# Kernel optimization log

Hardware: AMD Instinct MI355X
Metric: run time of the kernel (lower is better)

## Reference

```python
import jax, jax.numpy as jnp
import numpy as np

B, C, W, H = 32, 512, 28, 28  # input spatial = 2*init_width x 2*init_height
HEADS = 8


def setup_inputs() -> dict:
    key = jax.random.key(0)
    ks = jax.random.split(key, 9)
    d = C // HEADS
    s = 0.05
    return {
        "x": jax.random.normal(ks[0], (B, C, W, H), jnp.float32),
        # 1x1 conv weights == dense [out_c, in_c] + bias
        "wq": jax.random.normal(ks[1], (C, C), jnp.float32) * s,
        "bq": jax.random.normal(ks[2], (C,), jnp.float32) * s,
        "wk": jax.random.normal(ks[3], (C, C), jnp.float32) * s,
        "bk": jax.random.normal(ks[4], (C,), jnp.float32) * s,
        "wv": jax.random.normal(ks[5], (C, C), jnp.float32) * s,
        "bv": jax.random.normal(ks[6], (C,), jnp.float32) * s,
        "rel_h": jax.random.normal(ks[7], (1, HEADS, d, 1, H), jnp.float32),
        "rel_w": jax.random.normal(ks[8], (1, HEADS, d, W, 1), jnp.float32),
    }


def reference(x, wq, bq, wk, bk, wv, bv, rel_h, rel_w):
    b, c, w, h = x.shape
    heads = rel_h.shape[1]
    d = c // heads
    n = w * h

    def proj(wt, bi):
        # 1x1 conv == per-pixel dense over channels
        y = jnp.einsum('oc,bcwh->bowh', wt, x) + bi[None, :, None, None]
        return y.reshape(b, heads, d, n)  # [B, H, d, N]

    q = proj(wq, bq)
    k = proj(wk, bk)
    v = proj(wv, bv)

    # content-content: q^T k -> [B, H, N, N]
    cc = jnp.einsum('bhdn,bhdm->bhnm', q, k)
    # relative position bias: (rel_h + rel_w) broadcast to [H, d, 2w0*2h0] = [H, d, N]
    pos = (rel_h + rel_w).reshape(heads, d, n)
    # content-position: pos^T @ q -> [B, H, N, N]
    cp = jnp.einsum('hdp,bhdn->bhpn', pos, q)

    attn = jax.nn.softmax(cc + cp, axis=-1)  # softmax over last dim
    # out = v @ attn^T : [B, H, d, N]
    out = jnp.einsum('bhdn,bhmn->bhdm', v, attn)
    return out.reshape(b, c, w, h)
```

## Files before the change

### kernel.cpp

```cpp
#include <hip/hip_runtime.h>


#define BATCH 32
#define CCH   512
#define NHEAD 8
#define DH    64
#define NTOK  784
#define WSP   28
#define OT    128
#define NT    112
#define WLD   40
#define CH    64
#define NCHUNK 13
#define NIBLK  7
#define KQLD  136
#define VLD   72

typedef unsigned short u16;
typedef unsigned int   u32;
typedef short  short8  __attribute__((ext_vector_type(8)));
typedef float  floatx4 __attribute__((ext_vector_type(4)));

__device__ __forceinline__ u16 f2bf(float f) {
    union { float f; u32 i; } v; v.f = f;
    u32 x = v.i;
    return (u16)((x + 0x7FFFu + ((x >> 16) & 1u)) >> 16);
}
__device__ __forceinline__ u32 f2u(float f) { union { float f; u32 i; } v; v.f = f; return v.i; }
__device__ __forceinline__ float u2f(u32 u) { union { u32 i; float f; } v; v.i = u; return v.f; }

__device__ __forceinline__ u32 packsplit(float f) {
    const u32 hib = f2u(f) & 0xFFFF0000u;
    const float lo = f - u2f(hib);
    return ((u32)f2bf(lo) << 16) | (hib >> 16);
}

__global__ __launch_bounds__(256)
void pack_weights(const float* __restrict__ wq, const float* __restrict__ wk,
                  const float* __restrict__ wv,
                  u32* __restrict__ Wqp, u32* __restrict__ Wkp, u32* __restrict__ Wvp)
{
    const int i = blockIdx.x * 256 + threadIdx.x;
    if (i < CCH * CCH) {
        Wqp[i] = packsplit(wq[i]);
        Wkp[i] = packsplit(wk[i]);
        Wvp[i] = packsplit(wv[i]);
    }
}

__global__ __launch_bounds__(256)
void pack_x(const float* __restrict__ x, u32* __restrict__ Xp, int b0, size_t count)
{
    const size_t i = (size_t)blockIdx.x * 256 + threadIdx.x;
    if (i < count)
        Xp[i] = packsplit(x[(size_t)b0 * CCH * NTOK + i]);
}

__global__ __launch_bounds__(512, 4)
void qkv_proj(const u32* __restrict__ Xp,
              const u32* __restrict__ Wqp, const float* __restrict__ bq,
              const u32* __restrict__ Wkp, const float* __restrict__ bk,
              const u32* __restrict__ Wvp, const float* __restrict__ bv,
              u32* __restrict__ Qp, u32* __restrict__ Kp, u16* __restrict__ Vo,
              int nbatch)
{
    const int t    = threadIdx.x;
    const int lane = t & 63;
    const int wid  = t >> 6;
    const int z    = blockIdx.z;
    const int proj = z / nbatch;
    const int bl   = z - proj * nbatch;
    const int o0   = blockIdx.y * OT;
    const int n0   = blockIdx.x * NT;

    const u32*   Wp   = (proj == 0) ? Wqp : (proj == 1) ? Wkp : Wvp;
    const float* bias = (proj == 0) ? bq  : (proj == 1) ? bk  : bv;

    __shared__ u16 wh[OT][WLD], wl[OT][WLD];
    __shared__ u16 xh[NT][WLD], xl[NT][WLD];

    const int m    = lane & 15;
    const int quad = lane >> 4;

    floatx4 acc[7];
    #pragma unroll
    for (int j = 0; j < 7; j++) acc[j] = (floatx4){0.f, 0.f, 0.f, 0.f};

    const int wo = t >> 2;
    const int wc = (t & 3) * 8;
    const int xc = t >> 3;
    const int xn = (t & 7) * 14;

    const size_t xbase = (size_t)bl * CCH * NTOK;

    uint4 wv0, wv1;
    u32 xreg[14];
    {
        wv0 = *reinterpret_cast<const uint4*>(&Wp[(size_t)(o0 + wo) * CCH + 0 + wc]);
        wv1 = *reinterpret_cast<const uint4*>(&Wp[(size_t)(o0 + wo) * CCH + 0 + wc + 4]);
        if (t < 256) {
            #pragma unroll
            for (int u = 0; u < 7; u++) {
                const uint2 p = *reinterpret_cast<const uint2*>(&Xp[xbase + (size_t)(0 + xc) * NTOK + n0 + xn + 2 * u]);
                xreg[2 * u] = p.x; xreg[2 * u + 1] = p.y;
            }
        }
    }

    for (int c0 = 0; c0 < CCH; c0 += 32) {
        __syncthreads();
        {
            const u32 wr[8] = {wv0.x, wv0.y, wv0.z, wv0.w, wv1.x, wv1.y, wv1.z, wv1.w};
            ushort4 h0 = make_ushort4((u16)(wr[0] & 0xFFFF), (u16)(wr[1] & 0xFFFF), (u16)(wr[2] & 0xFFFF), (u16)(wr[3] & 0xFFFF));
            ushort4 h1 = make_ushort4((u16)(wr[4] & 0xFFFF), (u16)(wr[5] & 0xFFFF), (u16)(wr[6] & 0xFFFF), (u16)(wr[7] & 0xFFFF));
            ushort4 l0 = make_ushort4((u16)(wr[0] >> 16), (u16)(wr[1] >> 16), (u16)(wr[2] >> 16), (u16)(wr[3] >> 16));
            ushort4 l1 = make_ushort4((u16)(wr[4] >> 16), (u16)(wr[5] >> 16), (u16)(wr[6] >> 16), (u16)(wr[7] >> 16));
            *reinterpret_cast<ushort4*>(&wh[wo][wc])     = h0;
            *reinterpret_cast<ushort4*>(&wh[wo][wc + 4]) = h1;
            *reinterpret_cast<ushort4*>(&wl[wo][wc])     = l0;
            *reinterpret_cast<ushort4*>(&wl[wo][wc + 4]) = l1;
        }
        if (t < 256) {
            #pragma unroll
            for (int u = 0; u < 14; u++) {
                xh[xn + u][xc] = (u16)(xreg[u] & 0xFFFFu);
                xl[xn + u][xc] = (u16)(xreg[u] >> 16);
            }
        }
        __syncthreads();

        if (c0 + 32 < CCH) {
            wv0 = *reinterpret_cast<const uint4*>(&Wp[(size_t)(o0 + wo) * CCH + c0 + 32 + wc]);
            wv1 = *reinterpret_cast<const uint4*>(&Wp[(size_t)(o0 + wo) * CCH + c0 + 32 + wc + 4]);
            if (t < 256) {
                #pragma unroll
                for (int u = 0; u < 7; u++) {
                    const uint2 p = *reinterpret_cast<const uint2*>(&Xp[xbase + (size_t)(c0 + 32 + xc) * NTOK + n0 + xn + 2 * u]);
                    xreg[2 * u] = p.x; xreg[2 * u + 1] = p.y;
                }
            }
        }
        __builtin_amdgcn_sched_barrier(0);

        const short8 Ah = *reinterpret_cast<const short8*>(&wh[wid * 16 + m][quad * 8]);
        const short8 Al = *reinterpret_cast<const short8*>(&wl[wid * 16 + m][quad * 8]);
        #pragma unroll
        for (int jt = 0; jt < 7; jt++) {
            const short8 Bh = *reinterpret_cast<const short8*>(&xh[jt * 16 + m][quad * 8]);
            const short8 Bl = *reinterpret_cast<const short8*>(&xl[jt * 16 + m][quad * 8]);
            acc[jt] = __builtin_amdgcn_mfma_f32_16x16x32_bf16(Ah, Bh, acc[jt], 0, 0, 0);
            acc[jt] = __builtin_amdgcn_mfma_f32_16x16x32_bf16(Ah, Bl, acc[jt], 0, 0, 0);
            acc[jt] = __builtin_amdgcn_mfma_f32_16x16x32_bf16(Al, Bh, acc[jt], 0, 0, 0);
        }
    }

    const size_t obase = (size_t)bl * CCH * NTOK;
    #pragma unroll
    for (int r = 0; r < 4; r++) {
        const int o = o0 + wid * 16 + quad * 4 + r;
        const float bi = bias[o];
        #pragma unroll
        for (int jt = 0; jt < 7; jt++) {
            const int n = n0 + jt * 16 + m;
            const float val = acc[jt][r] + bi;
            const size_t idx = obase + (size_t)o * NTOK + n;
            if (proj == 0)      Qp[idx] = packsplit(val);
            else if (proj == 1) Kp[idx] = packsplit(val);
            else                Vo[idx] = f2bf(val);
        }
    }
}

__global__ __launch_bounds__(512)
void attn_kernel(const u32* __restrict__ Qp, const u32* __restrict__ Kp,
                 const u16* __restrict__ V,
                 const float* __restrict__ rel_h, const float* __restrict__ rel_w,
                 float* __restrict__ out, int b0)
{
    const int t    = threadIdx.x;
    const int lane = t & 63;
    const int wid  = t >> 6;
    const int m    = lane & 15;
    const int quad = lane >> 4;
    const int bl   = blockIdx.x;
    const int h    = blockIdx.y;
    int i0 = blockIdx.z * 128;
    if (i0 > NTOK - 128) i0 = NTOK - 128;
    const int b  = b0 + bl;
    const int hd = h * DH;
    const size_t base  = ((size_t)bl * CCH + hd) * NTOK;
    const size_t baseo = ((size_t)b  * CCH + hd) * NTOK;

    __shared__ u16 kqh[CH][KQLD];
    __shared__ u16 kql[CH][KQLD];
    __shared__ u16 vt[DH][VLD];
    __shared__ u16 pt[128][VLD];

    short8 Bh[4], Bl[4];
    {
        const int ig = i0 + wid * 16 + m;
        const int iw = ig / WSP, ih = ig % WSP;
        #pragma unroll
        for (int c = 0; c < 4; c++) {
            union { short8 v; u16 u[8]; } hb, lb;
            #pragma unroll
            for (int idx = 0; idx < 8; idx++) {
                const int k = c * 32 + quad * 8 + idx;
                if (k < DH) {
                    const u32 p = Qp[base + (size_t)k * NTOK + ig];
                    hb.u[idx] = (u16)(p & 0xFFFFu);
                    lb.u[idx] = (u16)(p >> 16);
                } else {
                    const int d = k - DH;
                    const float pos = rel_h[(size_t)(hd + d) * WSP + ih]
                                    + rel_w[(size_t)(hd + d) * WSP + iw];
                    const u32 hib = f2u(pos) & 0xFFFF0000u;
                    hb.u[idx] = (u16)(hib >> 16);
                    lb.u[idx] = f2bf(pos - u2f(hib));
                }
            }
            Bh[c] = hb.v; Bl[c] = lb.v;
        }
    }

    floatx4 Oacc[4];
    #pragma unroll
    for (int dt = 0; dt < 4; dt++) Oacc[dt] = (floatx4){0.f, 0.f, 0.f, 0.f};
    float mrun = -1e30f, lrun = 0.f;

    const int cg4 = (t & 31) * 4;
    const int jb4 = (t >> 5) * 4;
    const int vd  = t >> 3;
    const int vj  = (t & 7) * 8;

    for (int chn = 0; chn < NCHUNK; chn++) {
        const int j0 = chn * CH;
        __syncthreads();

        {
            u32 kv[4][4];
            #pragma unroll
            for (int cc = 0; cc < 4; cc++) {
                const int c = cg4 + cc;
                const u32* src = (c < DH) ? (Kp + base + (size_t)c * NTOK)
                                          : (Qp + base + (size_t)(c - DH) * NTOK);
                const uint4 a = *reinterpret_cast<const uint4*>(&src[j0 + jb4]);
                kv[cc][0] = a.x; kv[cc][1] = a.y; kv[cc][2] = a.z; kv[cc][3] = a.w;
            }
            #pragma unroll
            for (int jj = 0; jj < 4; jj++) {
                const ushort4 hi = make_ushort4((u16)(kv[0][jj] & 0xFFFFu), (u16)(kv[1][jj] & 0xFFFFu),
                                                (u16)(kv[2][jj] & 0xFFFFu), (u16)(kv[3][jj] & 0xFFFFu));
                const ushort4 lo = make_ushort4((u16)(kv[0][jj] >> 16), (u16)(kv[1][jj] >> 16),
                                                (u16)(kv[2][jj] >> 16), (u16)(kv[3][jj] >> 16));
                *reinterpret_cast<ushort4*>(&kqh[jb4 + jj][cg4]) = hi;
                *reinterpret_cast<ushort4*>(&kql[jb4 + jj][cg4]) = lo;
            }
        }
        if (j0 + vj + 8 <= NTOK) {
            const uint4 a = *reinterpret_cast<const uint4*>(&V[base + (size_t)vd * NTOK + j0 + vj]);
            *reinterpret_cast<uint4*>(&vt[vd][vj]) = a;
        } else {
            #pragma unroll
            for (int u = 0; u < 8; u++)
                vt[vd][vj + u] = (j0 + vj + u < NTOK) ? V[base + (size_t)vd * NTOK + j0 + vj + u] : (u16)0;
        }
        __syncthreads();

        floatx4 Sacc[4];
        #pragma unroll
        for (int js = 0; js < 4; js++) Sacc[js] = (floatx4){0.f, 0.f, 0.f, 0.f};
        #pragma unroll
        for (int c = 0; c < 4; c++) {
            #pragma unroll
            for (int js = 0; js < 4; js++) {
                const short8 Ah = *reinterpret_cast<const short8*>(&kqh[js * 16 + m][c * 32 + quad * 8]);
                const short8 Al = *reinterpret_cast<const short8*>(&kql[js * 16 + m][c * 32 + quad * 8]);
                Sacc[js] = __builtin_amdgcn_mfma_f32_16x16x32_bf16(Ah, Bh[c], Sacc[js], 0, 0, 0);
                Sacc[js] = __builtin_amdgcn_mfma_f32_16x16x32_bf16(Ah, Bl[c], Sacc[js], 0, 0, 0);
                Sacc[js] = __builtin_amdgcn_mfma_f32_16x16x32_bf16(Al, Bh[c], Sacc[js], 0, 0, 0);
            }
        }

        float sv[16];
        #pragma unroll
        for (int js = 0; js < 4; js++)
            #pragma unroll
            for (int r = 0; r < 4; r++) sv[js * 4 + r] = Sacc[js][r];
        if (j0 + CH > NTOK) {
            #pragma unroll
            for (int js = 0; js < 4; js++)
                #pragma unroll
                for (int r = 0; r < 4; r++)
                    if (j0 + js * 16 + quad * 4 + r >= NTOK) sv[js * 4 + r] = -1e30f;
        }
        float mc = sv[0];
        #pragma unroll
        for (int u = 1; u < 16; u++) mc = fmaxf(mc, sv[u]);
        mc = fmaxf(mc, __shfl_xor(mc, 16, 64));
        mc = fmaxf(mc, __shfl_xor(mc, 32, 64));
        const float mnew  = fmaxf(mrun, mc);
        const float alpha = __expf(mrun - mnew);
        float ps = 0.f;
        #pragma unroll
        for (int u = 0; u < 16; u++) {
            const float p = __expf(sv[u] - mnew);
            sv[u] = p;
            ps += p;
        }
        ps += __shfl_xor(ps, 16, 64);
        ps += __shfl_xor(ps, 32, 64);
        lrun = lrun * alpha + ps;
        mrun = mnew;
        #pragma unroll
        for (int dt = 0; dt < 4; dt++)
            #pragma unroll
            for (int r = 0; r < 4; r++) Oacc[dt][r] *= alpha;

        #pragma unroll
        for (int js = 0; js < 4; js++) {
            const ushort4 pw = make_ushort4(f2bf(sv[js * 4 + 0]), f2bf(sv[js * 4 + 1]),
                                            f2bf(sv[js * 4 + 2]), f2bf(sv[js * 4 + 3]));
            *reinterpret_cast<ushort4*>(&pt[wid * 16 + m][js * 16 + quad * 4]) = pw;
        }

        #pragma unroll
        for (int joff = 0; joff < CH; joff += 32) {
            const short8 Bp = *reinterpret_cast<const short8*>(&pt[wid * 16 + m][joff + quad * 8]);
            #pragma unroll
            for (int dt = 0; dt < 4; dt++) {
                const short8 Av = *reinterpret_cast<const short8*>(&vt[dt * 16 + m][joff + quad * 8]);
                Oacc[dt] = __builtin_amdgcn_mfma_f32_16x16x32_bf16(Av, Bp, Oacc[dt], 0, 0, 0);
            }
        }
    }

    const float linv = 1.f / lrun;
    #pragma unroll
    for (int dt = 0; dt < 4; dt++) {
        #pragma unroll
        for (int r = 0; r < 4; r++) {
            const int d = dt * 16 + quad * 4 + r;
            out[baseo + (size_t)d * NTOK + i0 + wid * 16 + m] = Oacc[dt][r] * linv;
        }
    }
}

extern "C" void kernel_launch(void* const* d_in, const int* in_sizes, int n_in,
                              void* d_out, int out_size, void* d_ws, size_t ws_size,
                              hipStream_t stream)
{
    const float* x  = (const float*)d_in[0];
    const float* wq = (const float*)d_in[1];
    const float* bq = (const float*)d_in[2];
    const float* wk = (const float*)d_in[3];
    const float* bk = (const float*)d_in[4];
    const float* wv = (const float*)d_in[5];
    const float* bv = (const float*)d_in[6];
    const float* rh = (const float*)d_in[7];
    const float* rw = (const float*)d_in[8];
    float* out = (float*)d_out;

    const size_t perB = (size_t)CCH * NTOK;
    const size_t WELEM = (size_t)CCH * CCH;
    const size_t weightBytes = 3 * WELEM * 4;
    const size_t perBatchBytes = perB * 14;

    size_t avail = (ws_size > weightBytes) ? (ws_size - weightBytes) : perBatchBytes;
    size_t nb_s = avail / perBatchBytes;
    int nb = (int)(nb_s < 1 ? 1 : (nb_s > BATCH ? BATCH : nb_s));

    u32* Wqp = (u32*)d_ws;
    u32* Wkp = Wqp + WELEM;
    u32* Wvp = Wkp + WELEM;
    u32* chunk0 = Wvp + WELEM;

    pack_weights<<<dim3((CCH * CCH + 255) / 256), dim3(256), 0, stream>>>(wq, wk, wv, Wqp, Wkp, Wvp);

    for (int b0 = 0; b0 < BATCH; b0 += nb) {
        const int curb = (BATCH - b0 < nb) ? (BATCH - b0) : nb;
        u32* Xp = chunk0;
        u32* Qp = Xp + (size_t)curb * perB;
        u32* Kp = Qp + (size_t)curb * perB;
        u16* Vb = (u16*)(Kp + (size_t)curb * perB);

        const size_t xcount = (size_t)curb * perB;
        pack_x<<<dim3((unsigned)((xcount + 255) / 256)), dim3(256), 0, stream>>>(x, Xp, b0, xcount);

        dim3 gp(NTOK / NT, CCH / OT, 3 * curb);
        qkv_proj<<<gp, dim3(512), 0, stream>>>(Xp, Wqp, bq, Wkp, bk, Wvp, bv,
                                               Qp, Kp, Vb, curb);

        dim3 ga(curb, NHEAD, NIBLK);
        attn_kernel<<<ga, dim3(512), 0, stream>>>(Qp, Kp, Vb, rh, rw, out, b0);
    }
}
```

Before: 525.6 us.

## Transpose packed X to token-major layout and skip low-weight MFMA for V

The X packing kernel now transposes x into an [N, C] token-major layout through a shared-memory tile. This lets the projection kernel load X with wide 16-byte vectors per row and write LDS with vector stores instead of scattered 2-byte stores. For the V projection, the weight low-part term (Al*Bh) and its LDS staging are skipped, since V is stored in bf16 anyway. This reduces MFMA count and LDS traffic for a third of the blocks, at the cost of slightly lower V precision and a transpose step in the pack kernel.

```diff
diff --git a/kernel.cpp b/kernel.cpp
--- a/kernel.cpp
+++ b/kernel.cpp
@@ -49,15 +49,38 @@
 }
 
 __global__ __launch_bounds__(256)
-void pack_x(const float* __restrict__ x, u32* __restrict__ Xp, int b0, size_t count)
+void pack_xt(const float* __restrict__ x, u32* __restrict__ Xt, int b0)
 {
-    const size_t i = (size_t)blockIdx.x * 256 + threadIdx.x;
-    if (i < count)
-        Xp[i] = packsplit(x[(size_t)b0 * CCH * NTOK + i]);
+    const int bl = blockIdx.z;
+    const int c0 = blockIdx.y * 32;
+    const int n0 = blockIdx.x * 32;
+    const int t  = threadIdx.x;
+    const int tn = t & 31;
+    const int tr = t >> 5;
+
+    __shared__ float tile[32][33];
+
+    const size_t xb = (size_t)(b0 + bl) * CCH * NTOK;
+    #pragma unroll
+    for (int k = 0; k < 4; k++) {
+        const int c = tr + k * 8;
+        const int n = n0 + tn;
+        if (n < NTOK)
+            tile[c][tn] = x[xb + (size_t)(c0 + c) * NTOK + n];
+    }
+    __syncthreads();
+    const size_t ob = (size_t)bl * NTOK * CCH;
+    #pragma unroll
+    for (int k = 0; k < 4; k++) {
+        const int n = n0 + tr + k * 8;
+        const int c = c0 + tn;
+        if (n < NTOK)
+            Xt[ob + (size_t)n * CCH + c] = packsplit(tile[tn][tr + k * 8]);
+    }
 }
 
 __global__ __launch_bounds__(512, 4)
-void qkv_proj(const u32* __restrict__ Xp,
+void qkv_proj(const u32* __restrict__ Xt,
               const u32* __restrict__ Wqp, const float* __restrict__ bq,
               const u32* __restrict__ Wkp, const float* __restrict__ bk,
               const u32* __restrict__ Wvp, const float* __restrict__ bv,
@@ -75,6 +98,7 @@
 
     const u32*   Wp   = (proj == 0) ? Wqp : (proj == 1) ? Wkp : Wvp;
     const float* bias = (proj == 0) ? bq  : (proj == 1) ? bk  : bv;
+    const bool   isV  = (proj == 2);
 
     __shared__ u16 wh[OT][WLD], wl[OT][WLD];
     __shared__ u16 xh[NT][WLD], xl[NT][WLD];
@@ -88,22 +112,18 @@
 
     const int wo = t >> 2;
     const int wc = (t & 3) * 8;
-    const int xc = t >> 3;
-    const int xn = (t & 7) * 14;
-
-    const size_t xbase = (size_t)bl * CCH * NTOK;
-
-    uint4 wv0, wv1;
-    u32 xreg[14];
+    const int xrow = t >> 2;
+    const int xc8  = (t & 3) * 8;
+
+    const size_t xtbase = (size_t)bl * NTOK * CCH;
+
+    uint4 wv0, wv1, xv0, xv1;
     {
         wv0 = *reinterpret_cast<const uint4*>(&Wp[(size_t)(o0 + wo) * CCH + 0 + wc]);
         wv1 = *reinterpret_cast<const uint4*>(&Wp[(size_t)(o0 + wo) * CCH + 0 + wc + 4]);
-        if (t < 256) {
-            #pragma unroll
-            for (int u = 0; u < 7; u++) {
-                const uint2 p = *reinterpret_cast<const uint2*>(&Xp[xbase + (size_t)(0 + xc) * NTOK + n0 + xn + 2 * u]);
-                xreg[2 * u] = p.x; xreg[2 * u + 1] = p.y;
-            }
+        if (t < 448) {
+            xv0 = *reinterpret_cast<const uint4*>(&Xt[xtbase + (size_t)(n0 + xrow) * CCH + 0 + xc8]);
+            xv1 = *reinterpret_cast<const uint4*>(&Xt[xtbase + (size_t)(n0 + xrow) * CCH + 0 + xc8 + 4]);
         }
     }
 
@@ -113,44 +133,49 @@
             const u32 wr[8] = {wv0.x, wv0.y, wv0.z, wv0.w, wv1.x, wv1.y, wv1.z, wv1.w};
             ushort4 h0 = make_ushort4((u16)(wr[0] & 0xFFFF), (u16)(wr[1] & 0xFFFF), (u16)(wr[2] & 0xFFFF), (u16)(wr[3] & 0xFFFF));
             ushort4 h1 = make_ushort4((u16)(wr[4] & 0xFFFF), (u16)(wr[5] & 0xFFFF), (u16)(wr[6] & 0xFFFF), (u16)(wr[7] & 0xFFFF));
-            ushort4 l0 = make_ushort4((u16)(wr[0] >> 16), (u16)(wr[1] >> 16), (u16)(wr[2] >> 16), (u16)(wr[3] >> 16));
-            ushort4 l1 = make_ushort4((u16)(wr[4] >> 16), (u16)(wr[5] >> 16), (u16)(wr[6] >> 16), (u16)(wr[7] >> 16));
             *reinterpret_cast<ushort4*>(&wh[wo][wc])     = h0;
             *reinterpret_cast<ushort4*>(&wh[wo][wc + 4]) = h1;
-            *reinterpret_cast<ushort4*>(&wl[wo][wc])     = l0;
-            *reinterpret_cast<ushort4*>(&wl[wo][wc + 4]) = l1;
-        }
-        if (t < 256) {
-            #pragma unroll
-            for (int u = 0; u < 14; u++) {
-                xh[xn + u][xc] = (u16)(xreg[u] & 0xFFFFu);
-                xl[xn + u][xc] = (u16)(xreg[u] >> 16);
-            }
+            if (!isV) {
+                ushort4 l0 = make_ushort4((u16)(wr[0] >> 16), (u16)(wr[1] >> 16), (u16)(wr[2] >> 16), (u16)(wr[3] >> 16));
+                ushort4 l1 = make_ushort4((u16)(wr[4] >> 16), (u16)(wr[5] >> 16), (u16)(wr[6] >> 16), (u16)(wr[7] >> 16));
+                *reinterpret_cast<ushort4*>(&wl[wo][wc])     = l0;
+                *reinterpret_cast<ushort4*>(&wl[wo][wc + 4]) = l1;
+            }
+        }
+        if (t < 448) {
+            const u32 xr[8] = {xv0.x, xv0.y, xv0.z, xv0.w, xv1.x, xv1.y, xv1.z, xv1.w};
+            ushort4 h0 = make_ushort4((u16)(xr[0] & 0xFFFF), (u16)(xr[1] & 0xFFFF), (u16)(xr[2] & 0xFFFF), (u16)(xr[3] & 0xFFFF));
+            ushort4 h1 = make_ushort4((u16)(xr[4] & 0xFFFF), (u16)(xr[5] & 0xFFFF), (u16)(xr[6] & 0xFFFF), (u16)(xr[7] & 0xFFFF));
+            ushort4 l0 = make_ushort4((u16)(xr[0] >> 16), (u16)(xr[1] >> 16), (u16)(xr[2] >> 16), (u16)(xr[3] >> 16));
+            ushort4 l1 = make_ushort4((u16)(xr[4] >> 16), (u16)(xr[5] >> 16), (u16)(xr[6] >> 16), (u16)(xr[7] >> 16));
+            *reinterpret_cast<ushort4*>(&xh[xrow][xc8])     = h0;
+            *reinterpret_cast<ushort4*>(&xh[xrow][xc8 + 4]) = h1;
+            *reinterpret_cast<ushort4*>(&xl[xrow][xc8])     = l0;
+            *reinterpret_cast<ushort4*>(&xl[xrow][xc8 + 4]) = l1;
         }
         __syncthreads();
 
         if (c0 + 32 < CCH) {
             wv0 = *reinterpret_cast<const uint4*>(&Wp[(size_t)(o0 + wo) * CCH + c0 + 32 + wc]);
             wv1 = *reinterpret_cast<const uint4*>(&Wp[(size_t)(o0 + wo) * CCH + c0 + 32 + wc + 4]);
-            if (t < 256) {
-                #pragma unroll
-                for (int u = 0; u < 7; u++) {
-                    const uint2 p = *reinterpret_cast<const uint2*>(&Xp[xbase + (size_t)(c0 + 32 + xc) * NTOK + n0 + xn + 2 * u]);
-                    xreg[2 * u] = p.x; xreg[2 * u + 1] = p.y;
-                }
+            if (t < 448) {
+                xv0 = *reinterpret_cast<const uint4*>(&Xt[xtbase + (size_t)(n0 + xrow) * CCH + c0 + 32 + xc8]);
+                xv1 = *reinterpret_cast<const uint4*>(&Xt[xtbase + (size_t)(n0 + xrow) * CCH + c0 + 32 + xc8 + 4]);
             }
         }
         __builtin_amdgcn_sched_barrier(0);
 
         const short8 Ah = *reinterpret_cast<const short8*>(&wh[wid * 16 + m][quad * 8]);
-        const short8 Al = *reinterpret_cast<const short8*>(&wl[wid * 16 + m][quad * 8]);
+        short8 Al{};
+        if (!isV) Al = *reinterpret_cast<const short8*>(&wl[wid * 16 + m][quad * 8]);
         #pragma unroll
         for (int jt = 0; jt < 7; jt++) {
             const short8 Bh = *reinterpret_cast<const short8*>(&xh[jt * 16 + m][quad * 8]);
             const short8 Bl = *reinterpret_cast<const short8*>(&xl[jt * 16 + m][quad * 8]);
             acc[jt] = __builtin_amdgcn_mfma_f32_16x16x32_bf16(Ah, Bh, acc[jt], 0, 0, 0);
             acc[jt] = __builtin_amdgcn_mfma_f32_16x16x32_bf16(Ah, Bl, acc[jt], 0, 0, 0);
-            acc[jt] = __builtin_amdgcn_mfma_f32_16x16x32_bf16(Al, Bh, acc[jt], 0, 0, 0);
+            if (!isV)
+                acc[jt] = __builtin_amdgcn_mfma_f32_16x16x32_bf16(Al, Bh, acc[jt], 0, 0, 0);
         }
     }
 
@@ -379,16 +404,16 @@
 
     for (int b0 = 0; b0 < BATCH; b0 += nb) {
         const int curb = (BATCH - b0 < nb) ? (BATCH - b0) : nb;
-        u32* Xp = chunk0;
-        u32* Qp = Xp + (size_t)curb * perB;
+        u32* Xt = chunk0;
+        u32* Qp = Xt + (size_t)curb * perB;
         u32* Kp = Qp + (size_t)curb * perB;
         u16* Vb = (u16*)(Kp + (size_t)curb * perB);
 
-        const size_t xcount = (size_t)curb * perB;
-        pack_x<<<dim3((unsigned)((xcount + 255) / 256)), dim3(256), 0, stream>>>(x, Xp, b0, xcount);
+        dim3 gx((NTOK + 31) / 32, CCH / 32, curb);
+        pack_xt<<<gx, dim3(256), 0, stream>>>(x, Xt, b0);
 
         dim3 gp(NTOK / NT, CCH / OT, 3 * curb);
-        qkv_proj<<<gp, dim3(512), 0, stream>>>(Xp, Wqp, bq, Wkp, bk, Wvp, bv,
+        qkv_proj<<<gp, dim3(512), 0, stream>>>(Xt, Wqp, bq, Wkp, bk, Wvp, bv,
                                                Qp, Kp, Vb, curb);
 
         dim3 ga(curb, NHEAD, NIBLK);
```

After: 512.3 us. -2.5%, faster.
